# Kernel tuning notes

Hardware: AMD Instinct MI355X
Metric: run time of the kernel (lower is better)

The kernel has to match this reference:

```python
import jax, jax.numpy as jnp
import numpy as np

B, T, D, H = 512, 512, 256, 512

def setup_inputs() -> dict:
    key = jax.random.key(0)
    ks = jax.random.split(key, 7)
    s_ih = 1.0 / np.sqrt(H)
    return {
        "x": jax.random.normal(ks[0], (B, T, D), dtype=jnp.float32),
        "W_ih": jax.random.normal(ks[1], (4 * H, D), dtype=jnp.float32) * s_ih,
        "W_hh": jax.random.normal(ks[2], (4 * H, H), dtype=jnp.float32) * s_ih,
        "b_ih": jax.random.normal(ks[3], (4 * H,), dtype=jnp.float32) * s_ih,
        "b_hh": jax.random.normal(ks[4], (4 * H,), dtype=jnp.float32) * s_ih,
        "W_fc": jax.random.normal(ks[5], (1, H), dtype=jnp.float32) * s_ih,
        "b_fc": jax.random.normal(ks[6], (1,), dtype=jnp.float32) * s_ih,
    }

def reference(x, W_ih, W_hh, b_ih, b_hh, W_fc, b_fc):
    # Precompute input projections for all steps: [T, B, 4H]
    xg = jnp.einsum('btd,gd->tbg', x, W_ih) + b_ih + b_hh

    def step(carry, xg_t):
        h, c = carry
        gates = xg_t + h @ W_hh.T  # [B, 4H]
        i, f, g, o = jnp.split(gates, 4, axis=-1)  # torch LSTMCell gate order
        i = jax.nn.sigmoid(i)
        f = jax.nn.sigmoid(f)
        g = jnp.tanh(g)
        o = jax.nn.sigmoid(o)
        c = f * c + i * g
        h = o * jnp.tanh(c)
        return (h, c), None

    h0 = jnp.zeros((x.shape[0], W_hh.shape[1]), dtype=x.dtype)
    (h, _), _ = jax.lax.scan(step, (h0, h0), xg)
    # dropout in eval mode is identity
    return jax.nn.sigmoid(h @ W_fc.T + b_fc)  # [B, 1]
```

## Files before the change

kernel.cpp:

```cpp
#include <hip/hip_runtime.h>

typedef _Float16 f16;
typedef _Float16 f16x8 __attribute__((ext_vector_type(8)));
typedef float f32x4 __attribute__((ext_vector_type(4)));
typedef unsigned int u32;
typedef unsigned long long u64;

#define TT 512
#define BB 512
#define DD 256
#define HH 512

#define WPACK_BYTES (32*4*24*64*8*2)
#define HBUF_OFF    (WPACK_BYTES)
#define FLAG_OFF    (HBUF_OFF + 2*BB*HH*2)
#define NFLAGS      ((TT+1)*8*4*32)

__device__ __forceinline__ float sigf(float v) {
    return __frcp_rn(1.0f + __expf(-v));
}
__device__ __forceinline__ float tanh_fast(float v) {
    float e = __expf(2.0f * fminf(v, 15.0f));
    return 1.0f - 2.0f * __frcp_rn(e + 1.0f);
}

__global__ void pack_w(const float* __restrict__ W_ih,
                       const float* __restrict__ W_hh,
                       f16* __restrict__ Wp) {
    int tid = blockIdx.x * 256 + threadIdx.x;
    if (tid >= 32*4*24*64) return;
    int lane = tid & 63;
    int rest = tid >> 6;
    int ks   = rest % 24;
    int t3   = rest / 24;
    int nt   = t3 & 3;
    int ji   = t3 >> 2;
    int g  = nt*512 + ji*16 + (lane & 15);
    int k0 = ks*32 + ((lane >> 4) & 3)*8;
    const float* src = (k0 < 256) ? (W_ih + (size_t)g*DD + k0)
                                  : (W_hh + (size_t)g*HH + (k0 - 256));
    f16x8 v;
    #pragma unroll
    for (int j = 0; j < 8; ++j) v[j] = (f16)src[j];
    *(f16x8*)(Wp + (size_t)tid*8) = v;
}

#define LDH16_SC1(A, p) asm volatile(                                  \
    "global_load_dwordx4 %0, %16, off sc1\n\t"                         \
    "global_load_dwordx4 %1, %16, off offset:64 sc1\n\t"               \
    "global_load_dwordx4 %2, %16, off offset:128 sc1\n\t"              \
    "global_load_dwordx4 %3, %16, off offset:192 sc1\n\t"              \
    "global_load_dwordx4 %4, %16, off offset:256 sc1\n\t"              \
    "global_load_dwordx4 %5, %16, off offset:320 sc1\n\t"              \
    "global_load_dwordx4 %6, %16, off offset:384 sc1\n\t"              \
    "global_load_dwordx4 %7, %16, off offset:448 sc1\n\t"              \
    "global_load_dwordx4 %8, %16, off offset:512 sc1\n\t"              \
    "global_load_dwordx4 %9, %16, off offset:576 sc1\n\t"              \
    "global_load_dwordx4 %10, %16, off offset:640 sc1\n\t"             \
    "global_load_dwordx4 %11, %16, off offset:704 sc1\n\t"             \
    "global_load_dwordx4 %12, %16, off offset:768 sc1\n\t"             \
    "global_load_dwordx4 %13, %16, off offset:832 sc1\n\t"             \
    "global_load_dwordx4 %14, %16, off offset:896 sc1\n\t"             \
    "global_load_dwordx4 %15, %16, off offset:960 sc1\n\t"             \
    "s_waitcnt vmcnt(0)"                                               \
    : "=&v"((A)[0]), "=&v"((A)[1]), "=&v"((A)[2]), "=&v"((A)[3]),      \
      "=&v"((A)[4]), "=&v"((A)[5]), "=&v"((A)[6]), "=&v"((A)[7]),      \
      "=&v"((A)[8]), "=&v"((A)[9]), "=&v"((A)[10]), "=&v"((A)[11]),    \
      "=&v"((A)[12]), "=&v"((A)[13]), "=&v"((A)[14]), "=&v"((A)[15])   \
    : "v"(p) : "memory")

__launch_bounds__(256, 1)
__global__ void lstm_fused(const float* __restrict__ x,
                           const float* __restrict__ b_ih,
                           const float* __restrict__ b_hh,
                           const float* __restrict__ W_fc,
                           const float* __restrict__ b_fc,
                           const f16* __restrict__ Wp,
                           f16* __restrict__ hbuf,
                           u32* __restrict__ flags,
                           float* __restrict__ out) {
    extern __shared__ char smem[];
    f16x8* Wlds = (f16x8*)smem;

    const int tid  = threadIdx.x;
    const int lane = tid & 63;
    const int w    = tid >> 6;
    const int bi   = blockIdx.x & 7;
    const int ji   = blockIdx.x >> 3;

    {
        const f16x8* src = (const f16x8*)Wp + (size_t)ji * (4*24*64);
        for (int i = tid; i < 4*24*64; i += 256) Wlds[i] = src[i];
    }

    const int uq = (lane >> 4) * 4;
    float bias[4][4];
    #pragma unroll
    for (int nt = 0; nt < 4; ++nt)
        #pragma unroll
        for (int r = 0; r < 4; ++r)
            bias[nt][r] = b_ih[nt*512 + ji*16 + uq + r] + b_hh[nt*512 + ji*16 + uq + r];
    __syncthreads();

    const int batch  = bi*64 + w*16 + (lane & 15);
    const int koff   = (lane >> 4) * 8;
    const float* xrow = x + (size_t)batch * TT * DD + koff;
    u64* hq = (u64*)hbuf;
    const int hrow_q = (batch * HH + koff) >> 2;
    u64* hdst0 = hq + ((batch * HH + ji*16 + uq) >> 2);

    float c[4] = {0.f, 0.f, 0.f, 0.f};
    f32x4 acc[4];

    {
        float4 xa[8], xb[8];
        #pragma unroll
        for (int ks = 0; ks < 8; ++ks) {
            xa[ks] = *(const float4*)(xrow + ks*32);
            xb[ks] = *(const float4*)(xrow + ks*32 + 4);
        }
        #pragma unroll
        for (int nt = 0; nt < 4; ++nt)
            acc[nt] = (f32x4){bias[nt][0], bias[nt][1], bias[nt][2], bias[nt][3]};
        #pragma unroll
        for (int ks = 0; ks < 8; ++ks) {
            f16x8 a;
            a[0]=(f16)xa[ks].x; a[1]=(f16)xa[ks].y; a[2]=(f16)xa[ks].z; a[3]=(f16)xa[ks].w;
            a[4]=(f16)xb[ks].x; a[5]=(f16)xb[ks].y; a[6]=(f16)xb[ks].z; a[7]=(f16)xb[ks].w;
            #pragma unroll
            for (int nt = 0; nt < 4; ++nt)
                acc[nt] = __builtin_amdgcn_mfma_f32_16x16x32_f16(
                    Wlds[(nt*24 + ks)*64 + lane], a, acc[nt], 0, 0, 0);
        }
    }

    for (int s = 0; s < TT; ++s) {
        if (s > 0) {
            const u32* f = flags + (((size_t)s*8 + bi)*4 + w)*32;
            for (;;) {
                u32 v = 1u;
                if (lane < 32)
                    v = __hip_atomic_load(&f[lane], __ATOMIC_RELAXED,
                                          __HIP_MEMORY_SCOPE_AGENT);
                if (__all(v != 0)) break;
                __builtin_amdgcn_s_sleep(1);
            }
            asm volatile("" ::: "memory");

            const size_t pbase = (size_t)(s & 1) * (BB*HH/4);
            f16x8 Ah[16];
            const u64* hb = hq + pbase + hrow_q;
            LDH16_SC1(Ah, hb);
            #pragma unroll
            for (int ks = 0; ks < 16; ++ks)
                #pragma unroll
                for (int nt = 0; nt < 4; ++nt)
                    acc[nt] = __builtin_amdgcn_mfma_f32_16x16x32_f16(
                        Wlds[(nt*24 + ks + 8)*64 + lane], Ah[ks], acc[nt], 0, 0, 0);
        }

        union { u64 q; f16 h4[4]; } H;
        #pragma unroll
        for (int r = 0; r < 4; ++r) {
            float ig = sigf(acc[0][r]);
            float fg = sigf(acc[1][r]);
            float gg = tanh_fast(acc[2][r]);
            float og = sigf(acc[3][r]);
            c[r] = fg * c[r] + ig * gg;
            H.h4[r] = (f16)(og * tanh_fast(c[r]));
        }
        __hip_atomic_store(hdst0 + (size_t)((s + 1) & 1) * (BB*HH/4), H.q,
                           __ATOMIC_RELAXED, __HIP_MEMORY_SCOPE_AGENT);

        asm volatile("s_waitcnt vmcnt(0)" ::: "memory");
        if (lane == 0)
            __hip_atomic_store(&flags[(((size_t)(s + 1)*8 + bi)*4 + w)*32 + ji],
                               1u, __ATOMIC_RELAXED, __HIP_MEMORY_SCOPE_AGENT);

        if (s + 1 < TT) {
            const float* xs = xrow + (size_t)(s + 1) * DD;
            float4 na[8], nb[8];
            #pragma unroll
            for (int ks = 0; ks < 8; ++ks) {
                na[ks] = *(const float4*)(xs + ks*32);
                nb[ks] = *(const float4*)(xs + ks*32 + 4);
            }
            #pragma unroll
            for (int nt = 0; nt < 4; ++nt)
                acc[nt] = (f32x4){bias[nt][0], bias[nt][1], bias[nt][2], bias[nt][3]};
            #pragma unroll
            for (int ks = 0; ks < 8; ++ks) {
                f16x8 a;
                a[0]=(f16)na[ks].x; a[1]=(f16)na[ks].y; a[2]=(f16)na[ks].z; a[3]=(f16)na[ks].w;
                a[4]=(f16)nb[ks].x; a[5]=(f16)nb[ks].y; a[6]=(f16)nb[ks].z; a[7]=(f16)nb[ks].w;
                #pragma unroll
                for (int nt = 0; nt < 4; ++nt)
                    acc[nt] = __builtin_amdgcn_mfma_f32_16x16x32_f16(
                        Wlds[(nt*24 + ks)*64 + lane], a, acc[nt], 0, 0, 0);
            }
        }
    }

    if (ji == 0) {
        {
            const u32* f = flags + (((size_t)TT*8 + bi)*4 + w)*32;
            for (;;) {
                u32 v = 1u;
                if (lane < 32)
                    v = __hip_atomic_load(&f[lane], __ATOMIC_RELAXED,
                                          __HIP_MEMORY_SCOPE_AGENT);
                if (__all(v != 0)) break;
                __builtin_amdgcn_s_sleep(1);
            }
        }
        asm volatile("" ::: "memory");
        __syncthreads();
        const u64* hT = hq + (size_t)(TT & 1) * (BB*HH/4);
        float* red = (float*)smem;
        int b_local = tid >> 2, seg = tid & 3;
        const u64* hr = hT + (((size_t)(bi*64 + b_local) * HH + seg*128) >> 2);
        const float* wf = W_fc + seg*128;
        float ssum = 0.f;
        for (int kq = 0; kq < 32; ++kq) {
            union { u64 q; f16 h4[4]; } Hv;
            Hv.q = __hip_atomic_load(hr + kq, __ATOMIC_RELAXED,
                                     __HIP_MEMORY_SCOPE_AGENT);
            #pragma unroll
            for (int j = 0; j < 4; ++j) ssum += (float)Hv.h4[j] * wf[kq*4 + j];
        }
        red[b_local*4 + seg] = ssum;
        __syncthreads();
        if (tid < 64) {
            float v = red[tid*4+0] + red[tid*4+1] + red[tid*4+2] + red[tid*4+3] + b_fc[0];
            out[bi*64 + tid] = sigf(v);
        }
    }
}

extern "C" void kernel_launch(void* const* d_in, const int* in_sizes, int n_in,
                              void* d_out, int out_size, void* d_ws, size_t ws_size,
                              hipStream_t stream) {
    const float* x    = (const float*)d_in[0];
    const float* W_ih = (const float*)d_in[1];
    const float* W_hh = (const float*)d_in[2];
    const float* b_ih = (const float*)d_in[3];
    const float* b_hh = (const float*)d_in[4];
    const float* W_fc = (const float*)d_in[5];
    const float* b_fc = (const float*)d_in[6];
    float* out = (float*)d_out;

    f16* Wp    = (f16*)d_ws;
    f16* hbuf  = (f16*)((char*)d_ws + HBUF_OFF);
    u32* flags = (u32*)((char*)d_ws + FLAG_OFF);

    hipMemsetAsync(flags, 0, NFLAGS * sizeof(u32), stream);
    pack_w<<<768, 256, 0, stream>>>(W_ih, W_hh, Wp);

    static bool attr_set = []() {
        hipFuncSetAttribute(reinterpret_cast<const void*>(lstm_fused),
                            hipFuncAttributeMaxDynamicSharedMemorySize, 98304);
        return true;
    }();
    (void)attr_set;

    void* kargs[] = {(void*)&x, (void*)&b_ih, (void*)&b_hh, (void*)&W_fc,
                     (void*)&b_fc, (void*)&Wp, (void*)&hbuf, (void*)&flags,
                     (void*)&out};
    hipError_t e = hipLaunchCooperativeKernel(
        reinterpret_cast<const void*>(lstm_fused),
        dim3(256), dim3(256), kargs, 98304, stream);
    if (e != hipSuccess) {
        lstm_fused<<<dim3(256), dim3(256), 98304, stream>>>(
            x, b_ih, b_hh, W_fc, b_fc, Wp, hbuf, flags, out);
    }
}
```

Before: 2.801 ms.

## Replace flag-based step sync with sentinel-valued hidden-state polling in 4-slot ring

```diff
diff --git a/kernel.cpp b/kernel.cpp
--- a/kernel.cpp
+++ b/kernel.cpp
@@ -4,6 +4,7 @@
 typedef _Float16 f16x8 __attribute__((ext_vector_type(8)));
 typedef float f32x4 __attribute__((ext_vector_type(4)));
 typedef unsigned int u32;
+typedef u32 u32x4 __attribute__((ext_vector_type(4)));
 typedef unsigned long long u64;
 
 #define TT 512
@@ -13,8 +14,8 @@
 
 #define WPACK_BYTES (32*4*24*64*8*2)
 #define HBUF_OFF    (WPACK_BYTES)
-#define FLAG_OFF    (HBUF_OFF + 2*BB*HH*2)
-#define NFLAGS      ((TT+1)*8*4*32)
+#define HQ_SLOT     (BB*HH/4)
+#define HBUF_BYTES  (4*BB*HH*2)
 
 __device__ __forceinline__ float sigf(float v) {
     return __frcp_rn(1.0f + __expf(-v));
@@ -69,6 +70,35 @@
       "=&v"((A)[12]), "=&v"((A)[13]), "=&v"((A)[14]), "=&v"((A)[15])   \
     : "v"(p) : "memory")
 
+#define LDH256_SC1(A, p) asm volatile(                                 \
+    "global_load_dwordx4 %0, %16, off sc1\n\t"                         \
+    "global_load_dwordx4 %1, %16, off offset:16 sc1\n\t"               \
+    "global_load_dwordx4 %2, %16, off offset:32 sc1\n\t"               \
+    "global_load_dwordx4 %3, %16, off offset:48 sc1\n\t"               \
+    "global_load_dwordx4 %4, %16, off offset:64 sc1\n\t"               \
+    "global_load_dwordx4 %5, %16, off offset:80 sc1\n\t"               \
+    "global_load_dwordx4 %6, %16, off offset:96 sc1\n\t"               \
+    "global_load_dwordx4 %7, %16, off offset:112 sc1\n\t"              \
+    "global_load_dwordx4 %8, %16, off offset:128 sc1\n\t"              \
+    "global_load_dwordx4 %9, %16, off offset:144 sc1\n\t"              \
+    "global_load_dwordx4 %10, %16, off offset:160 sc1\n\t"             \
+    "global_load_dwordx4 %11, %16, off offset:176 sc1\n\t"             \
+    "global_load_dwordx4 %12, %16, off offset:192 sc1\n\t"             \
+    "global_load_dwordx4 %13, %16, off offset:208 sc1\n\t"             \
+    "global_load_dwordx4 %14, %16, off offset:224 sc1\n\t"             \
+    "global_load_dwordx4 %15, %16, off offset:240 sc1\n\t"             \
+    "s_waitcnt vmcnt(0)"                                               \
+    : "=&v"((A)[0]), "=&v"((A)[1]), "=&v"((A)[2]), "=&v"((A)[3]),      \
+      "=&v"((A)[4]), "=&v"((A)[5]), "=&v"((A)[6]), "=&v"((A)[7]),      \
+      "=&v"((A)[8]), "=&v"((A)[9]), "=&v"((A)[10]), "=&v"((A)[11]),    \
+      "=&v"((A)[12]), "=&v"((A)[13]), "=&v"((A)[14]), "=&v"((A)[15])   \
+    : "v"(p) : "memory")
+
+__device__ __forceinline__ bool chunk_ok(const f16x8& c) {
+    u32x4 t = __builtin_bit_cast(u32x4, c);
+    return ((t.y >> 16) != 0xFFFFu) && ((t.w >> 16) != 0xFFFFu);
+}
+
 __launch_bounds__(256, 1)
 __global__ void lstm_fused(const float* __restrict__ x,
                            const float* __restrict__ b_ih,
@@ -77,7 +107,6 @@
                            const float* __restrict__ b_fc,
                            const f16* __restrict__ Wp,
                            f16* __restrict__ hbuf,
-                           u32* __restrict__ flags,
                            float* __restrict__ out) {
     extern __shared__ char smem[];
     f16x8* Wlds = (f16x8*)smem;
@@ -107,7 +136,7 @@
     const float* xrow = x + (size_t)batch * TT * DD + koff;
     u64* hq = (u64*)hbuf;
     const int hrow_q = (batch * HH + koff) >> 2;
-    u64* hdst0 = hq + ((batch * HH + ji*16 + uq) >> 2);
+    const int hoff_q = (batch * HH + ji*16 + uq) >> 2;
 
     float c[4] = {0.f, 0.f, 0.f, 0.f};
     f32x4 acc[4];
@@ -136,27 +165,30 @@
 
     for (int s = 0; s < TT; ++s) {
         if (s > 0) {
-            const u32* f = flags + (((size_t)s*8 + bi)*4 + w)*32;
+            const u64* hb = hq + (size_t)(s & 3) * HQ_SLOT + hrow_q;
+            f16x8 Ah[16];
             for (;;) {
-                u32 v = 1u;
-                if (lane < 32)
-                    v = __hip_atomic_load(&f[lane], __ATOMIC_RELAXED,
-                                          __HIP_MEMORY_SCOPE_AGENT);
-                if (__all(v != 0)) break;
-                __builtin_amdgcn_s_sleep(1);
+                LDH16_SC1(Ah, hb);
+                bool ok = true;
+                #pragma unroll
+                for (int ks = 0; ks < 16; ++ks) ok = ok && chunk_ok(Ah[ks]);
+                if (__all(ok)) break;
+                __builtin_amdgcn_s_sleep(2);
             }
-            asm volatile("" ::: "memory");
-
-            const size_t pbase = (size_t)(s & 1) * (BB*HH/4);
-            f16x8 Ah[16];
-            const u64* hb = hq + pbase + hrow_q;
-            LDH16_SC1(Ah, hb);
+            if (s + 3 <= TT)
+                __hip_atomic_store(hq + (size_t)((s + 3) & 3) * HQ_SLOT + hoff_q,
+                                   0xFFFFFFFFFFFFFFFFull, __ATOMIC_RELAXED,
+                                   __HIP_MEMORY_SCOPE_AGENT);
             #pragma unroll
             for (int ks = 0; ks < 16; ++ks)
                 #pragma unroll
                 for (int nt = 0; nt < 4; ++nt)
                     acc[nt] = __builtin_amdgcn_mfma_f32_16x16x32_f16(
                         Wlds[(nt*24 + ks + 8)*64 + lane], Ah[ks], acc[nt], 0, 0, 0);
+        } else {
+            __hip_atomic_store(hq + (size_t)3 * HQ_SLOT + hoff_q,
+                               0xFFFFFFFFFFFFFFFFull, __ATOMIC_RELAXED,
+                               __HIP_MEMORY_SCOPE_AGENT);
         }
 
         union { u64 q; f16 h4[4]; } H;
@@ -169,13 +201,10 @@
             c[r] = fg * c[r] + ig * gg;
             H.h4[r] = (f16)(og * tanh_fast(c[r]));
         }
-        __hip_atomic_store(hdst0 + (size_t)((s + 1) & 1) * (BB*HH/4), H.q,
+
+        asm volatile("s_waitcnt vmcnt(0)" ::: "memory");
+        __hip_atomic_store(hq + (size_t)((s + 1) & 3) * HQ_SLOT + hoff_q, H.q,
                            __ATOMIC_RELAXED, __HIP_MEMORY_SCOPE_AGENT);
-
-        asm volatile("s_waitcnt vmcnt(0)" ::: "memory");
-        if (lane == 0)
-            __hip_atomic_store(&flags[(((size_t)(s + 1)*8 + bi)*4 + w)*32 + ji],
-                               1u, __ATOMIC_RELAXED, __HIP_MEMORY_SCOPE_AGENT);
 
         if (s + 1 < TT) {
             const float* xs = xrow + (size_t)(s + 1) * DD;
@@ -202,33 +231,27 @@
     }
 
     if (ji == 0) {
-        {
-            const u32* f = flags + (((size_t)TT*8 + bi)*4 + w)*32;
-            for (;;) {
-                u32 v = 1u;
-                if (lane < 32)
-                    v = __hip_atomic_load(&f[lane], __ATOMIC_RELAXED,
-                                          __HIP_MEMORY_SCOPE_AGENT);
-                if (__all(v != 0)) break;
-                __builtin_amdgcn_s_sleep(1);
-            }
-        }
-        asm volatile("" ::: "memory");
+        const u64* hr = hq + (size_t)(TT & 3) * HQ_SLOT
+                      + (((size_t)(bi*64 + (tid >> 2)) * HH + (tid & 3)*128) >> 2);
+        f16x8 Hh[16];
+        for (;;) {
+            LDH256_SC1(Hh, hr);
+            bool ok = true;
+            #pragma unroll
+            for (int ks = 0; ks < 16; ++ks) ok = ok && chunk_ok(Hh[ks]);
+            if (__all(ok)) break;
+            __builtin_amdgcn_s_sleep(2);
+        }
+        const float* wf = W_fc + (tid & 3)*128;
+        float ssum = 0.f;
+        #pragma unroll
+        for (int c2 = 0; c2 < 16; ++c2)
+            #pragma unroll
+            for (int e = 0; e < 8; ++e)
+                ssum += (float)Hh[c2][e] * wf[c2*8 + e];
         __syncthreads();
-        const u64* hT = hq + (size_t)(TT & 1) * (BB*HH/4);
         float* red = (float*)smem;
-        int b_local = tid >> 2, seg = tid & 3;
-        const u64* hr = hT + (((size_t)(bi*64 + b_local) * HH + seg*128) >> 2);
-        const float* wf = W_fc + seg*128;
-        float ssum = 0.f;
-        for (int kq = 0; kq < 32; ++kq) {
-            union { u64 q; f16 h4[4]; } Hv;
-            Hv.q = __hip_atomic_load(hr + kq, __ATOMIC_RELAXED,
-                                     __HIP_MEMORY_SCOPE_AGENT);
-            #pragma unroll
-            for (int j = 0; j < 4; ++j) ssum += (float)Hv.h4[j] * wf[kq*4 + j];
-        }
-        red[b_local*4 + seg] = ssum;
+        red[(tid >> 2)*4 + (tid & 3)] = ssum;
         __syncthreads();
         if (tid < 64) {
             float v = red[tid*4+0] + red[tid*4+1] + red[tid*4+2] + red[tid*4+3] + b_fc[0];
@@ -249,11 +272,10 @@
     const float* b_fc = (const float*)d_in[6];
     float* out = (float*)d_out;
 
-    f16* Wp    = (f16*)d_ws;
-    f16* hbuf  = (f16*)((char*)d_ws + HBUF_OFF);
-    u32* flags = (u32*)((char*)d_ws + FLAG_OFF);
-
-    hipMemsetAsync(flags, 0, NFLAGS * sizeof(u32), stream);
+    f16* Wp   = (f16*)d_ws;
+    f16* hbuf = (f16*)((char*)d_ws + HBUF_OFF);
+
+    hipMemsetAsync(hbuf, 0xFF, HBUF_BYTES, stream);
     pack_w<<<768, 256, 0, stream>>>(W_ih, W_hh, Wp);
 
     static bool attr_set = []() {
@@ -264,13 +286,12 @@
     (void)attr_set;
 
     void* kargs[] = {(void*)&x, (void*)&b_ih, (void*)&b_hh, (void*)&W_fc,
-                     (void*)&b_fc, (void*)&Wp, (void*)&hbuf, (void*)&flags,
-                     (void*)&out};
+                     (void*)&b_fc, (void*)&Wp, (void*)&hbuf, (void*)&out};
     hipError_t e = hipLaunchCooperativeKernel(
         reinterpret_cast<const void*>(lstm_fused),
         dim3(256), dim3(256), kargs, 98304, stream);
     if (e != hipSuccess) {
         lstm_fused<<<dim3(256), dim3(256), 98304, stream>>>(
-            x, b_ih, b_hh, W_fc, b_fc, Wp, hbuf, flags, out);
-    }
-}
+            x, b_ih, b_hh, W_fc, b_fc, Wp, hbuf, out);
+    }
+}
```

Result: faster. 2.620 ms (median of 2 runs) (-6.5%).
